# Kernel tuning notes

Measured on AMD Instinct MI355X. Metric: run time of the kernel, lower is better.

## Reference

```python
import jax, jax.numpy as jnp
import numpy as np

F, B, H, N = 2048, 2, 1024, 16
E = H // N  # per-head depth = 64


def setup_inputs() -> dict:
    key = jax.random.key(0)
    k1, k2, k3, k4 = jax.random.split(key, 4)
    q_input = jax.random.normal(k1, (F, B, H), dtype=jnp.float32)
    mask = jax.random.randint(k2, (B, 1, F, F), 0, 2).astype(bool)
    w_qkv = jax.random.normal(k3, (H, 3 * H), dtype=jnp.float32) * 0.02
    b_qkv = jnp.zeros((3 * H,), dtype=jnp.float32)
    w_out = jax.random.normal(k4, (N, E, H), dtype=jnp.float32) * 0.02
    b_out = jnp.zeros((H,), dtype=jnp.float32)
    return {"q_input": q_input, "mask": mask, "w_qkv": w_qkv, "b_qkv": b_qkv,
            "w_out": w_out, "b_out": b_out}


def reference(q_input, mask, w_qkv, b_qkv, w_out, b_out):
    # fused QKV projection: FBH,HD->FBD (+ bias on D)
    qkv = jnp.einsum('fbh,hd->fbd', q_input, w_qkv) + b_qkv          # [F,B,3H]
    qkv = qkv.reshape(F, B, N, 3 * E)
    q, k, v = jnp.split(qkv, 3, axis=-1)                             # each [F,B,N,E]
    scale = 1.0 / jnp.sqrt(jnp.asarray(E, dtype=q.dtype))
    logits = jnp.einsum('fbne,tbne->bnft', q, k) * scale             # [B,N,F,T]
    logits = jnp.where(mask, logits, jnp.asarray(-10000.0, logits.dtype))
    attn_w = jax.nn.softmax(logits, axis=-1)
    ctx = jnp.einsum('bnft,tbne->bnfe', attn_w, v)                   # [B,N,F,E]
    ctx = jnp.transpose(ctx, (2, 0, 1, 3))                           # [F,B,N,E]
    out = jnp.einsum('fbne,ned->fbd', ctx, w_out)                    # [F,B,H] (no bias added)
    return out, b_out
```

## Files before the change

### kernel.cpp

```cpp
#include <hip/hip_runtime.h>
#include <hip/hip_bf16.h>
#include <math.h>

#define F_DIM 2048
#define B_DIM 2
#define H_DIM 1024
#define N_HEADS 16
#define E_DIM 64
#define D3 3072
#define M_DIM 4096

typedef __hip_bfloat16 bf16;
typedef __attribute__((ext_vector_type(8))) __bf16 bf16x8;
typedef __attribute__((ext_vector_type(8))) unsigned short u16x8;
typedef __attribute__((ext_vector_type(4))) float f32x4;

static __device__ __forceinline__ unsigned short f2bf(float f) {
    unsigned u = __float_as_uint(f);
    return (unsigned short)((u + 0x7FFFu + ((u >> 16) & 1u)) >> 16);
}

static __device__ __forceinline__ void glds16(const unsigned short* g, unsigned short* l) {
    __builtin_amdgcn_global_load_lds((const __attribute__((address_space(1))) unsigned int*)g,
                                     (__attribute__((address_space(3))) unsigned int*)l,
                                     16, 0, 0);
}

__global__ __launch_bounds__(256) void prep_kernel(const float* __restrict__ q_input,
                                                   const void* __restrict__ mask,
                                                   const float* __restrict__ w_qkv,
                                                   const float* __restrict__ w_out,
                                                   const float* __restrict__ b_out,
                                                   unsigned short* __restrict__ qin_bf,
                                                   unsigned short* __restrict__ wqkv_bt,
                                                   unsigned short* __restrict__ wout_bt,
                                                   unsigned* __restrict__ mbits,
                                                   float* __restrict__ bout_dst) {
    __shared__ float sh[32 * 33];
    const int bid = blockIdx.x;
    const int tid = threadIdx.x;

    if (bid < 2048) {
        int i = (bid * 256 + tid) * 8;
        float4 a = *(const float4*)&q_input[i];
        float4 b = *(const float4*)&q_input[i + 4];
        u16x8 o;
        o[0] = f2bf(a.x); o[1] = f2bf(a.y); o[2] = f2bf(a.z); o[3] = f2bf(a.w);
        o[4] = f2bf(b.x); o[5] = f2bf(b.y); o[6] = f2bf(b.z); o[7] = f2bf(b.w);
        *(u16x8*)&qin_bf[i] = o;
    } else if (bid < 6144) {
        const float* in; unsigned short* out; int R, C, bx, by;
        if (bid < 5120) { int idx = bid - 2048; in = w_qkv; out = wqkv_bt; R = 1024; C = 3072; bx = idx % 96; by = idx / 96; }
        else            { int idx = bid - 5120; in = w_out; out = wout_bt; R = 1024; C = 1024; bx = idx % 32; by = idx / 32; }
        float (*t)[33] = (float(*)[33])sh;
        const int c0 = bx * 32, r0 = by * 32;
        const int lc = tid & 31, lr = tid >> 5;
        #pragma unroll
        for (int i = 0; i < 4; ++i) {
            int r = lr + i * 8;
            t[r][lc] = in[(size_t)(r0 + r) * C + c0 + lc];
        }
        __syncthreads();
        #pragma unroll
        for (int i = 0; i < 4; ++i) {
            int r = lr + i * 8;
            out[(size_t)(c0 + r) * R + r0 + lc] = f2bf(t[lc][r]);
        }
    } else if (bid < 7168) {
        int* shi = (int*)sh;
        int v = ((const int*)mask)[tid] & ~1;
        unsigned long long bal = __ballot(v != 0);
        if ((tid & 63) == 0) shi[tid >> 6] = (bal != 0) ? 1 : 0;
        __syncthreads();
        const int byte_mode = shi[0] | shi[1] | shi[2] | shi[3];
        int w = (bid - 6144) * 256 + tid;
        size_t base = (size_t)w * 32;
        unsigned out = 0;
        if (byte_mode) {
            const unsigned char* mu = (const unsigned char*)mask;
            #pragma unroll
            for (int j = 0; j < 32; ++j) out |= (mu[base + j] ? 1u : 0u) << j;
        } else {
            const int* mi = (const int*)mask;
            #pragma unroll
            for (int j = 0; j < 32; ++j) out |= (mi[base + j] ? 1u : 0u) << j;
        }
        mbits[w] = out;
    } else {
        int h = (bid - 7168) * 256 + tid;
        if (h < H_DIM) bout_dst[h] = b_out[h];
    }
}

__global__ void detect_mask_kernel(const int* __restrict__ mask_words, int* __restrict__ flag) {
    __shared__ int red[256];
    int v = mask_words[threadIdx.x];
    red[threadIdx.x] = v & ~1;
    __syncthreads();
    for (int s = 128; s > 0; s >>= 1) {
        if (threadIdx.x < s) red[threadIdx.x] |= red[threadIdx.x + s];
        __syncthreads();
    }
    if (threadIdx.x == 0) *flag = (red[0] != 0) ? 1 : 0;
}

__global__ void pack_mask_kernel(const int* __restrict__ mi, const unsigned char* __restrict__ mu,
                                 const int* __restrict__ flag, unsigned* __restrict__ bits) {
    int w = blockIdx.x * 256 + threadIdx.x;
    size_t base = (size_t)w * 32;
    unsigned out = 0;
    if (*flag) {
        #pragma unroll
        for (int j = 0; j < 32; ++j) out |= (mu[base + j] ? 1u : 0u) << j;
    } else {
        #pragma unroll
        for (int j = 0; j < 32; ++j) out |= (mi[base + j] ? 1u : 0u) << j;
    }
    bits[w] = out;
}

__global__ __launch_bounds__(256) void convert_kernel(const float* __restrict__ in,
                                                      unsigned short* __restrict__ out) {
    int i = (blockIdx.x * 256 + threadIdx.x) * 8;
    float4 a = *(const float4*)&in[i];
    float4 b = *(const float4*)&in[i + 4];
    u16x8 o;
    o[0] = f2bf(a.x); o[1] = f2bf(a.y); o[2] = f2bf(a.z); o[3] = f2bf(a.w);
    o[4] = f2bf(b.x); o[5] = f2bf(b.y); o[6] = f2bf(b.z); o[7] = f2bf(b.w);
    *(u16x8*)&out[i] = o;
}

__global__ __launch_bounds__(256) void transpose_bf16_kernel(const float* __restrict__ in,
                                                             unsigned short* __restrict__ out,
                                                             int R, int C) {
    __shared__ float t[32][33];
    const int c0 = blockIdx.x * 32, r0 = blockIdx.y * 32;
    const int lc = threadIdx.x & 31, lr = threadIdx.x >> 5;
    #pragma unroll
    for (int i = 0; i < 4; ++i) {
        int r = lr + i * 8;
        t[r][lc] = in[(size_t)(r0 + r) * C + c0 + lc];
    }
    __syncthreads();
    #pragma unroll
    for (int i = 0; i < 4; ++i) {
        int r = lr + i * 8;
        out[(size_t)(c0 + r) * R + r0 + lc] = f2bf(t[lc][r]);
    }
}

__global__ void bout_copy_kernel(const float* __restrict__ b_out, float* __restrict__ dst) {
    int h = blockIdx.x * 256 + threadIdx.x;
    if (h < H_DIM) dst[h] = b_out[h];
}

template<int BM, int BN, bool ADD_BIAS, bool OUT_BF16>
__global__ __launch_bounds__(256) void gemm_bt_kernel(const unsigned short* __restrict__ A,
                                                      const unsigned short* __restrict__ Bt,
                                                      const float* __restrict__ bias,
                                                      void* __restrict__ Cout, int Nc) {
    __shared__ unsigned short Ald[BM * 32];
    __shared__ unsigned short Bld[BN * 32];
    constexpr int WM = BM / 2, WN = BN / 2;
    constexpr int MI = WM / 16, NI = WN / 16;
    constexpr int ACH = BM * 4;
    constexpr int TCH = (BM + BN) * 4;
    const int tid = threadIdx.x;
    const int wave = tid >> 6;
    const int lane = tid & 63;
    const int quad = lane >> 4;
    const int l16 = lane & 15;
    const int wm = (wave & 1) * WM;
    const int wn = (wave >> 1) * WN;
    const int m0 = blockIdx.y * BM;
    const int n0 = blockIdx.x * BN;

    f32x4 acc[MI][NI];
    #pragma unroll
    for (int i = 0; i < MI; ++i)
        #pragma unroll
        for (int j = 0; j < NI; ++j) acc[i][j] = (f32x4){0.f, 0.f, 0.f, 0.f};

    for (int k0 = 0; k0 < 1024; k0 += 32) {
        __syncthreads();
        #pragma unroll
        for (int rr = 0; rr < TCH / 256; ++rr) {
            const int chunk = rr * 256 + tid;
            const int wbase = (rr * 256 + wave * 64) * 8;
            if (chunk < ACH) {
                const int row = chunk >> 2, ko = (chunk & 3) * 8;
                glds16(&A[(size_t)(m0 + row) * 1024 + k0 + ko], &Ald[wbase]);
            } else {
                const int c2 = chunk - ACH;
                const int row = c2 >> 2, ko = (c2 & 3) * 8;
                glds16(&Bt[(size_t)(n0 + row) * 1024 + k0 + ko], &Bld[wbase - ACH * 8]);
            }
        }
        __syncthreads();

        bf16x8 af[MI], bfr[NI];
        #pragma unroll
        for (int i = 0; i < MI; ++i)
            af[i] = *(const bf16x8*)&Ald[(wm + i * 16 + l16) * 32 + quad * 8];
        #pragma unroll
        for (int j = 0; j < NI; ++j)
            bfr[j] = *(const bf16x8*)&Bld[(wn + j * 16 + l16) * 32 + quad * 8];
        #pragma unroll
        for (int mi = 0; mi < MI; ++mi)
            #pragma unroll
            for (int ni = 0; ni < NI; ++ni)
                acc[mi][ni] = __builtin_amdgcn_mfma_f32_16x16x32_bf16(af[mi], bfr[ni], acc[mi][ni], 0, 0, 0);
    }

    #pragma unroll
    for (int ni = 0; ni < NI; ++ni) {
        const int col = n0 + wn + ni * 16 + l16;
        const float bv = ADD_BIAS ? bias[col] : 0.f;
        #pragma unroll
        for (int mi = 0; mi < MI; ++mi) {
            const int rowb = m0 + wm + mi * 16 + quad * 4;
            #pragma unroll
            for (int r = 0; r < 4; ++r) {
                float v = acc[mi][ni][r] + bv;
                if (OUT_BF16) ((unsigned short*)Cout)[(size_t)(rowb + r) * Nc + col] = f2bf(v);
                else          ((float*)Cout)[(size_t)(rowb + r) * Nc + col] = v;
            }
        }
    }
}

#define LSTR 72
__global__ __launch_bounds__(512) void attn_mfma_kernel(const bf16* __restrict__ qkv_,
                                                        const unsigned* __restrict__ mbits,
                                                        unsigned short* __restrict__ ctxb) {
    __shared__ unsigned short K_lds[64 * LSTR];
    __shared__ unsigned short Vt_lds[64 * LSTR];
    __shared__ unsigned short P_lds[128 * LSTR];

    const unsigned short* qkv = (const unsigned short*)qkv_;
    const int tid = threadIdx.x;
    const int wave = tid >> 6;
    const int lane = tid & 63;
    const int quad = lane >> 4;
    const int l16 = lane & 15;
    const int f0 = blockIdx.x * 128;
    const int b = blockIdx.y >> 4;
    const int n = blockIdx.y & 15;
    const int head = n * 192;

    bf16x8 qf[2];
    #pragma unroll
    for (int ks = 0; ks < 2; ++ks) {
        int f = f0 + wave * 16 + l16;
        qf[ks] = *(const bf16x8*)&qkv[(size_t)(f * B_DIM + b) * D3 + head + ks * 32 + quad * 8];
    }

    f32x4 O[4];
    #pragma unroll
    for (int ec = 0; ec < 4; ++ec) O[ec] = (f32x4){0.f, 0.f, 0.f, 0.f};
    float lsum[4] = {0.f, 0.f, 0.f, 0.f};

    unsigned short* Pw = P_lds + wave * 16 * LSTR;
    const float c_exp = 0.18033688011112042f;

    for (int t0 = 0; t0 < F_DIM; t0 += 64) {
        __syncthreads();

        {
            int tr = tid >> 3, e0 = (tid & 7) * 8;
            u16x8 kv = *(const u16x8*)&qkv[(size_t)((t0 + tr) * B_DIM + b) * D3 + head + 64 + e0];
            *(u16x8*)&K_lds[tr * LSTR + e0] = kv;
        }
        if (tid < 256) {
            int u = tid & 15, h = (tid >> 4) & 1, e0 = (tid >> 5) * 8;
            int ta = t0 + h * 32 + u;
            u16x8 v0 = *(const u16x8*)&qkv[(size_t)(ta * B_DIM + b) * D3 + head + 128 + e0];
            u16x8 v1 = *(const u16x8*)&qkv[(size_t)((ta + 16) * B_DIM + b) * D3 + head + 128 + e0];
            #pragma unroll
            for (int j = 0; j < 8; ++j) {
                unsigned pk = (unsigned)v0[j] | ((unsigned)v1[j] << 16);
                *(unsigned*)&Vt_lds[(e0 + j) * LSTR + h * 32 + 2 * u] = pk;
            }
        }
        __syncthreads();

        f32x4 S[4];
        #pragma unroll
        for (int ck = 0; ck < 4; ++ck) S[ck] = (f32x4){0.f, 0.f, 0.f, 0.f};
        #pragma unroll
        for (int ck = 0; ck < 4; ++ck) {
            bf16x8 kb0 = *(const bf16x8*)&K_lds[(ck * 16 + l16) * LSTR + quad * 8];
            bf16x8 kb1 = *(const bf16x8*)&K_lds[(ck * 16 + l16) * LSTR + 32 + quad * 8];
            S[ck] = __builtin_amdgcn_mfma_f32_16x16x32_bf16(qf[0], kb0, S[ck], 0, 0, 0);
            S[ck] = __builtin_amdgcn_mfma_f32_16x16x32_bf16(qf[1], kb1, S[ck], 0, 0, 0);
        }

        #pragma unroll
        for (int r = 0; r < 4; ++r) {
            const int row = quad * 4 + r;
            const int f = f0 + wave * 16 + row;
            uint2 wb = *(const uint2*)&mbits[((size_t)b * F_DIM + f) * 64 + (t0 >> 5)];
            float p[4];
            #pragma unroll
            for (int ck = 0; ck < 4; ++ck) {
                unsigned wsel = (ck & 2) ? wb.y : wb.x;
                int bit = ((ck & 1) << 4) + l16;
                float pv = __builtin_amdgcn_exp2f(S[ck][r] * c_exp);
                p[ck] = ((wsel >> bit) & 1u) ? pv : 0.f;
            }
            lsum[r] += (p[0] + p[1]) + (p[2] + p[3]);
            unsigned pk01 = (unsigned)f2bf(p[0]) | ((unsigned)f2bf(p[1]) << 16);
            unsigned pk23 = (unsigned)f2bf(p[2]) | ((unsigned)f2bf(p[3]) << 16);
            *(unsigned*)&Pw[row * LSTR + 2 * l16] = pk01;
            *(unsigned*)&Pw[row * LSTR + 32 + 2 * l16] = pk23;
        }

        #pragma unroll
        for (int ks = 0; ks < 2; ++ks) {
            bf16x8 pa = *(const bf16x8*)&Pw[l16 * LSTR + ks * 32 + quad * 8];
            #pragma unroll
            for (int ec = 0; ec < 4; ++ec) {
                bf16x8 vb = *(const bf16x8*)&Vt_lds[(ec * 16 + l16) * LSTR + ks * 32 + quad * 8];
                O[ec] = __builtin_amdgcn_mfma_f32_16x16x32_bf16(pa, vb, O[ec], 0, 0, 0);
            }
        }
    }

    #pragma unroll
    for (int r = 0; r < 4; ++r) {
        float l = lsum[r];
        #pragma unroll
        for (int d = 1; d < 16; d <<= 1) l += __shfl_xor(l, d);
        const int f = f0 + wave * 16 + quad * 4 + r;
        const float inv = 1.0f / l;
        #pragma unroll
        for (int ec = 0; ec < 4; ++ec) {
            ctxb[(size_t)(f * B_DIM + b) * H_DIM + n * 64 + ec * 16 + l16] = f2bf(O[ec][r] * inv);
        }
    }
}

extern "C" void kernel_launch(void* const* d_in, const int* in_sizes, int n_in,
                              void* d_out, int out_size, void* d_ws, size_t ws_size,
                              hipStream_t stream) {
    const float* q_input = (const float*)d_in[0];
    const void*  mask    = d_in[1];
    const float* w_qkv   = (const float*)d_in[2];
    const float* b_qkv   = (const float*)d_in[3];
    const float* w_out   = (const float*)d_in[4];
    const float* b_out   = (const float*)d_in[5];
    float* out = (float*)d_out;
    char* ws = (char*)d_ws;

    const size_t FUSED_WS = 25165824ull + 8388608 + 6291456 + 2097152 + 1048576;

    if (ws_size >= FUSED_WS) {
        bf16*           qkv     = (bf16*)ws;
        unsigned short* qin_bf  = (unsigned short*)(ws + 25165824);
        unsigned short* ctx     = qin_bf;
        unsigned short* wqkv_bt = (unsigned short*)(ws + 33554432);
        unsigned short* wout_bt = (unsigned short*)(ws + 39845888);
        unsigned*       mbits   = (unsigned*)(ws + 41943040);

        prep_kernel<<<7172, 256, 0, stream>>>(q_input, mask, w_qkv, w_out, b_out,
                                              qin_bf, wqkv_bt, wout_bt, mbits,
                                              out + (size_t)M_DIM * H_DIM);
        gemm_bt_kernel<128, 128, true, true><<<dim3(24, 32), 256, 0, stream>>>(qin_bf, wqkv_bt, b_qkv, qkv, 3072);
        attn_mfma_kernel<<<dim3(16, 32), 512, 0, stream>>>(qkv, mbits, ctx);
        gemm_bt_kernel<64, 128, false, false><<<dim3(8, 64), 256, 0, stream>>>(ctx, wout_bt, nullptr, out, 1024);
    } else {
        bf16*           qkv     = (bf16*)ws;
        unsigned short* qin_bf  = (unsigned short*)(ws + 25165824);
        unsigned short* ctx     = qin_bf;
        unsigned short* wqkv_bt = (unsigned short*)(ws + 33554432);
        unsigned short* wout_bt = wqkv_bt;
        unsigned*       mbits   = (unsigned*)(ws + 39845888);
        int*            flag    = (int*)(ws + 40894464);

        detect_mask_kernel<<<1, 256, 0, stream>>>((const int*)mask, flag);
        pack_mask_kernel<<<1024, 256, 0, stream>>>((const int*)mask, (const unsigned char*)mask, flag, mbits);
        convert_kernel<<<2048, 256, 0, stream>>>(q_input, qin_bf);
        transpose_bf16_kernel<<<dim3(96, 32), 256, 0, stream>>>(w_qkv, wqkv_bt, 1024, 3072);
        gemm_bt_kernel<128, 128, true, true><<<dim3(24, 32), 256, 0, stream>>>(qin_bf, wqkv_bt, b_qkv, qkv, 3072);
        transpose_bf16_kernel<<<dim3(32, 32), 256, 0, stream>>>(w_out, wout_bt, 1024, 1024);
        attn_mfma_kernel<<<dim3(16, 32), 512, 0, stream>>>(qkv, mbits, ctx);
        gemm_bt_kernel<64, 128, false, false><<<dim3(8, 64), 256, 0, stream>>>(ctx, wout_bt, nullptr, out, 1024);
        bout_copy_kernel<<<4, 256, 0, stream>>>(b_out, out + (size_t)M_DIM * H_DIM);
    }
}
```

Measured before the change: 239.2 us.

## Split attention over two key-range halves and combine partial results

Adds a templated split mode to the attention kernel: the key/value range is divided into two halves along a new grid z-dimension. Each half writes unnormalized partial outputs in bf16 plus partial row sums, and a new combine kernel adds them and normalizes. This doubles the number of attention blocks so more of the GPU's CUs stay busy. The cost is an extra kernel launch, extra global traffic for the partial buffers, and some precision loss from storing unnormalized partials in bf16. The split path is used only when the workspace is large enough.

```diff
diff --git a/kernel.cpp b/kernel.cpp
--- a/kernel.cpp
+++ b/kernel.cpp
@@ -18,6 +18,9 @@
 static __device__ __forceinline__ unsigned short f2bf(float f) {
     unsigned u = __float_as_uint(f);
     return (unsigned short)((u + 0x7FFFu + ((u >> 16) & 1u)) >> 16);
+}
+static __device__ __forceinline__ float bf2f(unsigned short b) {
+    return __uint_as_float(((unsigned)b) << 16);
 }
 
 static __device__ __forceinline__ void glds16(const unsigned short* g, unsigned short* l) {
@@ -230,9 +233,11 @@
 }
 
 #define LSTR 72
+template<bool SPLIT>
 __global__ __launch_bounds__(512) void attn_mfma_kernel(const bf16* __restrict__ qkv_,
                                                         const unsigned* __restrict__ mbits,
-                                                        unsigned short* __restrict__ ctxb) {
+                                                        unsigned short* __restrict__ outp,
+                                                        float* __restrict__ lpart) {
     __shared__ unsigned short K_lds[64 * LSTR];
     __shared__ unsigned short Vt_lds[64 * LSTR];
     __shared__ unsigned short P_lds[128 * LSTR];
@@ -247,6 +252,8 @@
     const int b = blockIdx.y >> 4;
     const int n = blockIdx.y & 15;
     const int head = n * 192;
+    const int tbase = SPLIT ? blockIdx.z * 1024 : 0;
+    const int tend  = SPLIT ? tbase + 1024 : F_DIM;
 
     bf16x8 qf[2];
     #pragma unroll
@@ -263,7 +270,7 @@
     unsigned short* Pw = P_lds + wave * 16 * LSTR;
     const float c_exp = 0.18033688011112042f;
 
-    for (int t0 = 0; t0 < F_DIM; t0 += 64) {
+    for (int t0 = tbase; t0 < tend; t0 += 64) {
         __syncthreads();
 
         {
@@ -332,12 +339,34 @@
         #pragma unroll
         for (int d = 1; d < 16; d <<= 1) l += __shfl_xor(l, d);
         const int f = f0 + wave * 16 + quad * 4 + r;
-        const float inv = 1.0f / l;
-        #pragma unroll
-        for (int ec = 0; ec < 4; ++ec) {
-            ctxb[(size_t)(f * B_DIM + b) * H_DIM + n * 64 + ec * 16 + l16] = f2bf(O[ec][r] * inv);
-        }
-    }
+        if (SPLIT) {
+            unsigned short* Op = outp + (size_t)blockIdx.z * 4194304;
+            #pragma unroll
+            for (int ec = 0; ec < 4; ++ec)
+                Op[(size_t)(f * B_DIM + b) * H_DIM + n * 64 + ec * 16 + l16] = f2bf(O[ec][r]);
+            if (l16 == 0) lpart[blockIdx.z * 65536 + (f * B_DIM + b) * 16 + n] = l;
+        } else {
+            const float inv = 1.0f / l;
+            #pragma unroll
+            for (int ec = 0; ec < 4; ++ec)
+                outp[(size_t)(f * B_DIM + b) * H_DIM + n * 64 + ec * 16 + l16] = f2bf(O[ec][r] * inv);
+        }
+    }
+}
+
+__global__ __launch_bounds__(256) void combine_kernel(const unsigned short* __restrict__ Opart,
+                                                      const float* __restrict__ lpart,
+                                                      unsigned short* __restrict__ ctx) {
+    int i = (blockIdx.x * 256 + threadIdx.x) * 8;
+    int row = i >> 10;
+    int n = (i & 1023) >> 6;
+    float inv = 1.0f / (lpart[row * 16 + n] + lpart[65536 + row * 16 + n]);
+    u16x8 a = *(const u16x8*)&Opart[i];
+    u16x8 c = *(const u16x8*)&Opart[4194304 + i];
+    u16x8 o;
+    #pragma unroll
+    for (int j = 0; j < 8; ++j) o[j] = f2bf((bf2f(a[j]) + bf2f(c[j])) * inv);
+    *(u16x8*)&ctx[i] = o;
 }
 
 extern "C" void kernel_launch(void* const* d_in, const int* in_sizes, int n_in,
@@ -352,7 +381,8 @@
     float* out = (float*)d_out;
     char* ws = (char*)d_ws;
 
-    const size_t FUSED_WS = 25165824ull + 8388608 + 6291456 + 2097152 + 1048576;
+    const size_t FUSED_WS = 42991616;
+    const size_t SPLIT_WS = 60293120;
 
     if (ws_size >= FUSED_WS) {
         bf16*           qkv     = (bf16*)ws;
@@ -366,7 +396,15 @@
                                               qin_bf, wqkv_bt, wout_bt, mbits,
                                               out + (size_t)M_DIM * H_DIM);
         gemm_bt_kernel<128, 128, true, true><<<dim3(24, 32), 256, 0, stream>>>(qin_bf, wqkv_bt, b_qkv, qkv, 3072);
-        attn_mfma_kernel<<<dim3(16, 32), 512, 0, stream>>>(qkv, mbits, ctx);
+
+        if (ws_size >= SPLIT_WS) {
+            unsigned short* Opart = (unsigned short*)(ws + 42991616);
+            float*          lpart = (float*)(ws + 59768832);
+            attn_mfma_kernel<true><<<dim3(16, 32, 2), 512, 0, stream>>>(qkv, mbits, Opart, lpart);
+            combine_kernel<<<2048, 256, 0, stream>>>(Opart, lpart, ctx);
+        } else {
+            attn_mfma_kernel<false><<<dim3(16, 32), 512, 0, stream>>>(qkv, mbits, ctx, nullptr);
+        }
         gemm_bt_kernel<64, 128, false, false><<<dim3(8, 64), 256, 0, stream>>>(ctx, wout_bt, nullptr, out, 1024);
     } else {
         bf16*           qkv     = (bf16*)ws;
@@ -383,7 +421,7 @@
         transpose_bf16_kernel<<<dim3(96, 32), 256, 0, stream>>>(w_qkv, wqkv_bt, 1024, 3072);
         gemm_bt_kernel<128, 128, true, true><<<dim3(24, 32), 256, 0, stream>>>(qin_bf, wqkv_bt, b_qkv, qkv, 3072);
         transpose_bf16_kernel<<<dim3(32, 32), 256, 0, stream>>>(w_out, wout_bt, 1024, 1024);
-        attn_mfma_kernel<<<dim3(16, 32), 512, 0, stream>>>(qkv, mbits, ctx);
+        attn_mfma_kernel<false><<<dim3(16, 32), 512, 0, stream>>>(qkv, mbits, ctx, nullptr);
         gemm_bt_kernel<64, 128, false, false><<<dim3(8, 64), 256, 0, stream>>>(ctx, wout_bt, nullptr, out, 1024);
         bout_copy_kernel<<<4, 256, 0, stream>>>(b_out, out + (size_t)M_DIM * H_DIM);
     }
```

Result: slower. 261.3 us (+9.3%).
